# Optimization experiments

Hardware: AMD Instinct MI355X
Metric: run time of the kernel (lower is better)

## Reference

```python
import jax, jax.numpy as jnp
import numpy as np

WORD_THRES = 0.2
COS_EPS = 1e-8
NEG_INF = -1e9


def setup_inputs() -> dict:
    key = jax.random.key(0)
    k1, k2, k3, k4 = jax.random.split(key, 4)
    B, L, V, E, A = 1024, 256, 50000, 300, 30
    inputs = jax.random.randint(k1, (B, L), 0, V)            # token ids, 0 == pad
    w_emb = jax.random.normal(k2, (V, E), dtype=jnp.float32) * 0.1
    a_emb = jax.random.normal(k3, (A, E), dtype=jnp.float32)
    a_weight = jax.random.uniform(k4, (A,), dtype=jnp.float32)
    return {"inputs": inputs, "w_emb": w_emb, "a_emb": a_emb, "a_weight": a_weight}


def reference(inputs, w_emb, a_emb, a_weight):
    # inputs: [B, L] int ids; w_emb: [V, E]; a_emb: [A, E]; a_weight: [A]
    inputs_len = (inputs != 0).sum(axis=1).astype(jnp.float32)      # [B]
    x_wrd = w_emb[inputs]                                            # [B, L, E]

    # cosine similarity between each aspect and each word (torch semantics:
    # dot / (max(||a||, eps) * max(||x||, eps)))
    a_norm = jnp.maximum(jnp.linalg.norm(a_emb, axis=-1), COS_EPS)   # [A]
    x_norm = jnp.maximum(jnp.linalg.norm(x_wrd, axis=-1), COS_EPS)   # [B, L]
    dot = jnp.einsum("ae,ble->abl", a_emb, x_wrd)                    # [A, B, L]
    sim = dot / (a_norm[:, None, None] * x_norm[None, :, :])

    # Threshold(word_thres, 0): x if x > thres else 0, then scale by aspect weight
    sim = jnp.where(sim > WORD_THRES, sim, 0.0) * a_weight[:, None, None]

    # centroid score: relu(sim).max over aspects, summed over seq, length-normalized
    centroid = jnp.maximum(sim, 0.0).max(axis=0)                     # [B, L]
    centroid_score = centroid.sum(axis=1) / (inputs_len + 1e-5)      # [B]

    # attention: mask exact zeros to -1e9, max over aspects, softmax over seq
    sim_m = jnp.where(sim == 0.0, NEG_INF, sim)
    scores = sim_m.max(axis=0)                                       # [B, L]
    a = jax.nn.softmax(scores, axis=1)                               # [B, L]

    z = jnp.einsum("bl,ble->be", a, x_wrd)                           # [B, E]
    enc_out = z * (centroid_score > 1e-4).astype(z.dtype)[:, None]
    return enc_out, a, centroid_score
```

## Files before the change

### kernel.cpp

```cpp
#include <hip/hip_runtime.h>
#include <math.h>

#define BB 1024
#define LL 256
#define VV 50000
#define EE 300
#define AA 30
#define WORD_THRES 0.2f
#define COS_EPS_F 1e-8f
#define NEG_INF_F -1e9f
#define RECHECK_DELTA 2e-4f

typedef __attribute__((ext_vector_type(8))) short bf16x8;
typedef __attribute__((ext_vector_type(4))) float f32x4;

#define MFMA16(a, b, c) __builtin_amdgcn_mfma_f32_16x16x32_bf16((a), (b), (c), 0, 0, 0)

__device__ __forceinline__ void gld_lds16(const float* g, float* l) {
    typedef const __attribute__((address_space(1))) void* gas_p;
    typedef __attribute__((address_space(3))) void* las_p;
    __builtin_amdgcn_global_load_lds((gas_p)g, (las_p)l, 16, 0, 0);
}

__device__ __forceinline__ unsigned pack_hi(float a, float b) {
    return (__float_as_uint(a) >> 16) | (__float_as_uint(b) & 0xFFFF0000u);
}
__device__ __forceinline__ float hi_part(float a) {
    return __uint_as_float(__float_as_uint(a) & 0xFFFF0000u);
}
__device__ __forceinline__ void cvt_hilo(const float4 f0, const float4 f1,
                                         uint4& uh, uint4& ul) {
    uh.x = pack_hi(f0.x, f0.y);
    uh.y = pack_hi(f0.z, f0.w);
    uh.z = pack_hi(f1.x, f1.y);
    uh.w = pack_hi(f1.z, f1.w);
    const float l0 = f0.x - hi_part(f0.x), l1 = f0.y - hi_part(f0.y);
    const float l2 = f0.z - hi_part(f0.z), l3 = f0.w - hi_part(f0.w);
    const float l4 = f1.x - hi_part(f1.x), l5 = f1.y - hi_part(f1.y);
    const float l6 = f1.z - hi_part(f1.z), l7 = f1.w - hi_part(f1.w);
    ul.x = pack_hi(l0, l1);
    ul.y = pack_hi(l2, l3);
    ul.z = pack_hi(l4, l5);
    ul.w = pack_hi(l6, l7);
}

__global__ void __launch_bounds__(128) cent_kernel(
    const float* __restrict__ w_emb,
    const float* __restrict__ a_emb,
    const float* __restrict__ a_weight,
    float* __restrict__ cent)
{
    __shared__ float4 s_a4[2400];
    __shared__ uint4 s_bfrag[40 * 64];
    __shared__ float s_scale[32];
    __shared__ float s_aw[32];

    const int t = threadIdx.x;
    const int l = t & 63;
    const int w = t >> 6;
    const int m = l & 15;
    const int kg = l >> 4;
    float* s_af = (float*)s_a4;

    {
        const float* gbase = w_emb + (size_t)blockIdx.x * 32 * EE;
        const float* gend = w_emb + (size_t)VV * EE;
#pragma unroll
        for (int i = 0; i < 19; ++i) {
            if (i < 18 || t < 96) {
                const int off = i * 512 + t * 4;
                const float* src = gbase + off;
                if (src > gend - 4) src = gend - 4;
                gld_lds16(src, s_af + off);
            }
        }
    }

    {
        const int a = t >> 2, j = t & 3;
        if (a < AA) {
            const float4* a4 = (const float4*)a_emb + a * 75;
            float n2a = 0.f;
            for (int c = j; c < 75; c += 4) {
                const float4 x = a4[c];
                n2a += x.x * x.x + x.y * x.y + x.z * x.z + x.w * x.w;
            }
            n2a += __shfl_xor(n2a, 1);
            n2a += __shfl_xor(n2a, 2);
            if (j == 0) {
                s_scale[a] = 1.f / fmaxf(sqrtf(n2a), COS_EPS_F);
                s_aw[a] = a_weight[a];
            }
        }
        if (t == 30 || t == 31) { s_scale[t] = 0.f; s_aw[t] = 0.f; }
    }

    for (int ks = w; ks < 10; ks += 2) {
        const int kb = kg * 8 + 32 * ks;
#pragma unroll
        for (int tt = 0; tt < 2; ++tt) {
            const int col = tt * 16 + m;
            float4 f0 = {0.f, 0.f, 0.f, 0.f}, f1 = {0.f, 0.f, 0.f, 0.f};
            if (col < AA) {
                const float* ap = a_emb + col * EE;
                if (kb <= 296) f0 = *(const float4*)(ap + kb);
                if (kb <= 292) f1 = *(const float4*)(ap + kb + 4);
            }
            uint4 uh, ul;
            cvt_hilo(f0, f1, uh, ul);
            s_bfrag[(ks * 4 + tt * 2 + 0) * 64 + l] = uh;
            s_bfrag[(ks * 4 + tt * 2 + 1) * 64 + l] = ul;
        }
    }

    asm volatile("s_waitcnt vmcnt(0)" ::: "memory");
    __syncthreads();

    const int vtile = blockIdx.x * 32 + w * 16;
    const float* __restrict__ arow = s_af + (w * 16 + m) * EE;

    f32x4 acc0 = {0.f, 0.f, 0.f, 0.f};
    f32x4 acc1 = {0.f, 0.f, 0.f, 0.f};
    float n2 = 0.f;
    const uint4* __restrict__ bp0 = s_bfrag + l;

#pragma unroll
    for (int i = 0; i < 10; ++i) {
        const int kb = kg * 8 + 32 * i;
        float4 f0 = *(const float4*)(arow + kb);
        float4 f1 = *(const float4*)(arow + kb + 4);
        if (i == 9) {
            const float4 z = {0.f, 0.f, 0.f, 0.f};
            if (kg >= 2) f0 = z;
            if (kg >= 1) f1 = z;
        }
        n2 = fmaf(f0.x, f0.x, fmaf(f0.y, f0.y, fmaf(f0.z, f0.z, fmaf(f0.w, f0.w, n2))));
        n2 = fmaf(f1.x, f1.x, fmaf(f1.y, f1.y, fmaf(f1.z, f1.z, fmaf(f1.w, f1.w, n2))));
        uint4 uh, ul;
        cvt_hilo(f0, f1, uh, ul);
        const bf16x8 ah = __builtin_bit_cast(bf16x8, uh);
        const bf16x8 al = __builtin_bit_cast(bf16x8, ul);
        const uint4* bp = bp0 + i * 256;
        const bf16x8 bh0 = __builtin_bit_cast(bf16x8, bp[0]);
        const bf16x8 bl0 = __builtin_bit_cast(bf16x8, bp[64]);
        const bf16x8 bh1 = __builtin_bit_cast(bf16x8, bp[128]);
        const bf16x8 bl1 = __builtin_bit_cast(bf16x8, bp[192]);
        acc0 = MFMA16(ah, bh0, acc0);
        acc1 = MFMA16(ah, bh1, acc1);
        acc0 = MFMA16(ah, bl0, acc0);
        acc1 = MFMA16(ah, bl1, acc1);
        acc0 = MFMA16(al, bh0, acc0);
        acc1 = MFMA16(al, bh1, acc1);
    }

    n2 += __shfl_xor(n2, 16);
    n2 += __shfl_xor(n2, 32);

    const float sc0 = s_scale[m], aw0 = s_aw[m];
    const float sc1 = s_scale[16 + m], aw1 = s_aw[16 + m];
    const bool col1ok = (16 + m) < AA;
    float mx[4];
#pragma unroll
    for (int j = 0; j < 4; ++j) {
        const int r = kg * 4 + j;
        const float n2r = __int_as_float(
            __builtin_amdgcn_ds_bpermute(r << 2, __float_as_int(n2)));
        const float inv_x = 1.f / fmaxf(sqrtf(n2r), COS_EPS_F);
        float c0 = acc0[j] * sc0 * inv_x;
        float c1 = acc1[j] * sc1 * inv_x;
        if (fabsf(c0 - WORD_THRES) < RECHECK_DELTA) {
            const float* wr = s_af + (w * 16 + r) * EE;
            const float* ar = a_emb + m * EE;
            float d = 0.f;
            for (int k = 0; k < EE; ++k) d = fmaf(wr[k], ar[k], d);
            c0 = d * sc0 * inv_x;
        }
        if (col1ok && fabsf(c1 - WORD_THRES) < RECHECK_DELTA) {
            const float* wr = s_af + (w * 16 + r) * EE;
            const float* ar = a_emb + (16 + m) * EE;
            float d = 0.f;
            for (int k = 0; k < EE; ++k) d = fmaf(wr[k], ar[k], d);
            c1 = d * sc1 * inv_x;
        }
        float mj = fmaxf((c0 > WORD_THRES) ? c0 * aw0 : 0.f,
                         (c1 > WORD_THRES) ? c1 * aw1 : 0.f);
        mj = fmaxf(mj, __shfl_xor(mj, 1));
        mj = fmaxf(mj, __shfl_xor(mj, 2));
        mj = fmaxf(mj, __shfl_xor(mj, 4));
        mj = fmaxf(mj, __shfl_xor(mj, 8));
        mx[j] = mj;
    }
    if (m == 0 && vtile < VV) {
        const float4 o = {mx[0], mx[1], mx[2], mx[3]};
        *(float4*)(cent + vtile + kg * 4) = o;
    }
}

__global__ void __launch_bounds__(256) row_kernel(
    const int* __restrict__ inputs,
    const float* __restrict__ w_emb,
    const float* __restrict__ cent,
    float* __restrict__ out)
{
    const int w = threadIdx.x >> 6;
    const int lane = threadIdx.x & 63;
    const int b = blockIdx.x * 4 + w;

    __shared__ int s_id[4][LL];
    __shared__ float s_w[4][LL];
    __shared__ int s_n[4];

    if (lane == 0) s_n[w] = 0;

    const int4 id4 = *(const int4*)(inputs + b * LL + lane * 4);
    const float c0 = cent[id4.x];
    const float c1 = cent[id4.y];
    const float c2 = cent[id4.z];
    const float c3 = cent[id4.w];
    const float sc0 = (c0 > 0.f) ? c0 : NEG_INF_F;
    const float sc1 = (c1 > 0.f) ? c1 : NEG_INF_F;
    const float sc2 = (c2 > 0.f) ? c2 : NEG_INF_F;
    const float sc3 = (c3 > 0.f) ? c3 : NEG_INF_F;

    float s1 = c0 + c1 + c2 + c3;
    float s2 = (id4.x != 0 ? 1.f : 0.f) + (id4.y != 0 ? 1.f : 0.f) +
               (id4.z != 0 ? 1.f : 0.f) + (id4.w != 0 ? 1.f : 0.f);
    float s3 = fmaxf(fmaxf(sc0, sc1), fmaxf(sc2, sc3));
#pragma unroll
    for (int o = 1; o < 64; o <<= 1) {
        s1 += __shfl_xor(s1, o);
        s2 += __shfl_xor(s2, o);
        s3 = fmaxf(s3, __shfl_xor(s3, o));
    }
    const float mx = s3;

    const float p0 = expf(sc0 - mx);
    const float p1 = expf(sc1 - mx);
    const float p2 = expf(sc2 - mx);
    const float p3 = expf(sc3 - mx);
    float s4 = p0 + p1 + p2 + p3;
#pragma unroll
    for (int o = 1; o < 64; o <<= 1) s4 += __shfl_xor(s4, o);

    const float rinv = 1.f / s4;
    const float4 av = {p0 * rinv, p1 * rinv, p2 * rinv, p3 * rinv};
    *(float4*)(out + BB * EE + b * LL + lane * 4) = av;

    const float cs = s1 / (s2 + 1e-5f);
    const float gate = (cs > 1e-4f) ? 1.f : 0.f;
    if (lane == 0) out[BB * EE + BB * LL + b] = cs;

    if (sc0 > -1e8f) { const int i = atomicAdd(&s_n[w], 1); s_id[w][i] = id4.x; s_w[w][i] = av.x; }
    if (sc1 > -1e8f) { const int i = atomicAdd(&s_n[w], 1); s_id[w][i] = id4.y; s_w[w][i] = av.y; }
    if (sc2 > -1e8f) { const int i = atomicAdd(&s_n[w], 1); s_id[w][i] = id4.z; s_w[w][i] = av.z; }
    if (sc3 > -1e8f) { const int i = atomicAdd(&s_n[w], 1); s_id[w][i] = id4.w; s_w[w][i] = av.w; }
    __syncthreads();
    const int n = s_n[w];

    float4 accA = {0.f, 0.f, 0.f, 0.f};
    float4 accB = {0.f, 0.f, 0.f, 0.f};
    for (int i = 0; i < n; ++i) {
        const float wgt = s_w[w][i];
        const float4* rp = (const float4*)(w_emb + (size_t)s_id[w][i] * EE);
        const float4 ra = rp[lane];
        accA.x += wgt * ra.x; accA.y += wgt * ra.y;
        accA.z += wgt * ra.z; accA.w += wgt * ra.w;
        if (lane < 11) {
            const float4 rb = rp[64 + lane];
            accB.x += wgt * rb.x; accB.y += wgt * rb.y;
            accB.z += wgt * rb.z; accB.w += wgt * rb.w;
        }
    }
    accA.x *= gate; accA.y *= gate; accA.z *= gate; accA.w *= gate;
    *(float4*)(out + b * EE + 4 * lane) = accA;
    if (lane < 11) {
        accB.x *= gate; accB.y *= gate; accB.z *= gate; accB.w *= gate;
        *(float4*)(out + b * EE + 256 + 4 * lane) = accB;
    }
}

extern "C" void kernel_launch(void* const* d_in, const int* in_sizes, int n_in,
                              void* d_out, int out_size, void* d_ws, size_t ws_size,
                              hipStream_t stream) {
    const int* inputs = (const int*)d_in[0];
    const float* w_emb = (const float*)d_in[1];
    const float* a_emb = (const float*)d_in[2];
    const float* a_weight = (const float*)d_in[3];
    float* out = (float*)d_out;
    float* cent = (float*)d_ws;

    cent_kernel<<<(VV + 31) / 32, 128, 0, stream>>>(w_emb, a_emb, a_weight, cent);
    row_kernel<<<BB / 4, 256, 0, stream>>>(inputs, w_emb, cent, out);
}
```

Measured before the change: 135.8 us.

## Make centroid kernel persistent with double-buffered LDS staging and register-resident aspect fragments

The centroid kernel becomes a persistent grid of 256 blocks, one per CU, each looping over 64-row vocab tiles. Each wave stages the next tile into a second LDS buffer with async global-to-LDS loads while it computes the current one. The aspect B fragments are converted once and kept in registers, so they are no longer reread from LDS on every tile. This removes per-block launch and setup cost and hides load latency, but leaves only one block per CU and puts heavy pressure on registers and LDS.

```diff
diff --git a/kernel.cpp b/kernel.cpp
--- a/kernel.cpp
+++ b/kernel.cpp
@@ -10,6 +10,8 @@
 #define COS_EPS_F 1e-8f
 #define NEG_INF_F -1e9f
 #define RECHECK_DELTA 2e-4f
+#define CGRID 256
+#define NTILES 782
 
 typedef __attribute__((ext_vector_type(8))) short bf16x8;
 typedef __attribute__((ext_vector_type(4))) float f32x4;
@@ -44,14 +46,29 @@
     ul.w = pack_hi(l6, l7);
 }
 
-__global__ void __launch_bounds__(128) cent_kernel(
+__device__ __forceinline__ void stage16(const float* __restrict__ w_emb,
+                                        int tile, int w, int lane, float* dst) {
+    const float* gend = w_emb + (size_t)VV * EE - 4;
+    const float* g = w_emb + ((size_t)tile * 64 + w * 16) * EE;
+    float* d = dst + w * 4800;
+#pragma unroll
+    for (int i = 0; i < 19; ++i) {
+        if (i < 18 || lane < 48) {
+            const int off = i * 256 + lane * 4;
+            const float* src = g + off;
+            if (src > gend) src = gend;
+            gld_lds16(src, d + off);
+        }
+    }
+}
+
+__global__ void __launch_bounds__(256, 1) cent_kernel(
     const float* __restrict__ w_emb,
     const float* __restrict__ a_emb,
     const float* __restrict__ a_weight,
     float* __restrict__ cent)
 {
-    __shared__ float4 s_a4[2400];
-    __shared__ uint4 s_bfrag[40 * 64];
+    __shared__ uint4 s_pool[9600];
     __shared__ float s_scale[32];
     __shared__ float s_aw[32];
 
@@ -60,33 +77,19 @@
     const int w = t >> 6;
     const int m = l & 15;
     const int kg = l >> 4;
-    float* s_af = (float*)s_a4;
 
     {
-        const float* gbase = w_emb + (size_t)blockIdx.x * 32 * EE;
-        const float* gend = w_emb + (size_t)VV * EE;
-#pragma unroll
-        for (int i = 0; i < 19; ++i) {
-            if (i < 18 || t < 96) {
-                const int off = i * 512 + t * 4;
-                const float* src = gbase + off;
-                if (src > gend - 4) src = gend - 4;
-                gld_lds16(src, s_af + off);
-            }
-        }
-    }
-
-    {
-        const int a = t >> 2, j = t & 3;
+        const int a = t >> 3, j = t & 7;
         if (a < AA) {
             const float4* a4 = (const float4*)a_emb + a * 75;
             float n2a = 0.f;
-            for (int c = j; c < 75; c += 4) {
+            for (int c = j; c < 75; c += 8) {
                 const float4 x = a4[c];
                 n2a += x.x * x.x + x.y * x.y + x.z * x.z + x.w * x.w;
             }
             n2a += __shfl_xor(n2a, 1);
             n2a += __shfl_xor(n2a, 2);
+            n2a += __shfl_xor(n2a, 4);
             if (j == 0) {
                 s_scale[a] = 1.f / fmaxf(sqrtf(n2a), COS_EPS_F);
                 s_aw[a] = a_weight[a];
@@ -95,104 +98,122 @@
         if (t == 30 || t == 31) { s_scale[t] = 0.f; s_aw[t] = 0.f; }
     }
 
-    for (int ks = w; ks < 10; ks += 2) {
-        const int kb = kg * 8 + 32 * ks;
-#pragma unroll
-        for (int tt = 0; tt < 2; ++tt) {
-            const int col = tt * 16 + m;
-            float4 f0 = {0.f, 0.f, 0.f, 0.f}, f1 = {0.f, 0.f, 0.f, 0.f};
-            if (col < AA) {
-                const float* ap = a_emb + col * EE;
-                if (kb <= 296) f0 = *(const float4*)(ap + kb);
-                if (kb <= 292) f1 = *(const float4*)(ap + kb + 4);
-            }
-            uint4 uh, ul;
-            cvt_hilo(f0, f1, uh, ul);
-            s_bfrag[(ks * 4 + tt * 2 + 0) * 64 + l] = uh;
-            s_bfrag[(ks * 4 + tt * 2 + 1) * 64 + l] = ul;
-        }
-    }
-
-    asm volatile("s_waitcnt vmcnt(0)" ::: "memory");
+    {
+        uint4* s_bfrag = s_pool;
+        for (int ks = w; ks < 10; ks += 4) {
+            const int kb = kg * 8 + 32 * ks;
+#pragma unroll
+            for (int tt = 0; tt < 2; ++tt) {
+                const int col = tt * 16 + m;
+                float4 f0 = {0.f, 0.f, 0.f, 0.f}, f1 = {0.f, 0.f, 0.f, 0.f};
+                if (col < AA) {
+                    const float* ap = a_emb + col * EE;
+                    if (kb <= 296) f0 = *(const float4*)(ap + kb);
+                    if (kb <= 292) f1 = *(const float4*)(ap + kb + 4);
+                }
+                uint4 uh, ul;
+                cvt_hilo(f0, f1, uh, ul);
+                s_bfrag[(ks * 4 + tt * 2 + 0) * 64 + l] = uh;
+                s_bfrag[(ks * 4 + tt * 2 + 1) * 64 + l] = ul;
+            }
+        }
+    }
     __syncthreads();
 
-    const int vtile = blockIdx.x * 32 + w * 16;
-    const float* __restrict__ arow = s_af + (w * 16 + m) * EE;
-
-    f32x4 acc0 = {0.f, 0.f, 0.f, 0.f};
-    f32x4 acc1 = {0.f, 0.f, 0.f, 0.f};
-    float n2 = 0.f;
-    const uint4* __restrict__ bp0 = s_bfrag + l;
-
-#pragma unroll
-    for (int i = 0; i < 10; ++i) {
-        const int kb = kg * 8 + 32 * i;
-        float4 f0 = *(const float4*)(arow + kb);
-        float4 f1 = *(const float4*)(arow + kb + 4);
-        if (i == 9) {
-            const float4 z = {0.f, 0.f, 0.f, 0.f};
-            if (kg >= 2) f0 = z;
-            if (kg >= 1) f1 = z;
-        }
-        n2 = fmaf(f0.x, f0.x, fmaf(f0.y, f0.y, fmaf(f0.z, f0.z, fmaf(f0.w, f0.w, n2))));
-        n2 = fmaf(f1.x, f1.x, fmaf(f1.y, f1.y, fmaf(f1.z, f1.z, fmaf(f1.w, f1.w, n2))));
-        uint4 uh, ul;
-        cvt_hilo(f0, f1, uh, ul);
-        const bf16x8 ah = __builtin_bit_cast(bf16x8, uh);
-        const bf16x8 al = __builtin_bit_cast(bf16x8, ul);
-        const uint4* bp = bp0 + i * 256;
-        const bf16x8 bh0 = __builtin_bit_cast(bf16x8, bp[0]);
-        const bf16x8 bl0 = __builtin_bit_cast(bf16x8, bp[64]);
-        const bf16x8 bh1 = __builtin_bit_cast(bf16x8, bp[128]);
-        const bf16x8 bl1 = __builtin_bit_cast(bf16x8, bp[192]);
-        acc0 = MFMA16(ah, bh0, acc0);
-        acc1 = MFMA16(ah, bh1, acc1);
-        acc0 = MFMA16(ah, bl0, acc0);
-        acc1 = MFMA16(ah, bl1, acc1);
-        acc0 = MFMA16(al, bh0, acc0);
-        acc1 = MFMA16(al, bh1, acc1);
-    }
-
-    n2 += __shfl_xor(n2, 16);
-    n2 += __shfl_xor(n2, 32);
+    bf16x8 bfr[40];
+#pragma unroll
+    for (int q = 0; q < 40; ++q)
+        bfr[q] = __builtin_bit_cast(bf16x8, s_pool[q * 64 + l]);
+    __syncthreads();
+
+    float* buf0 = (float*)s_pool;
+    float* buf1 = buf0 + 19200;
 
     const float sc0 = s_scale[m], aw0 = s_aw[m];
     const float sc1 = s_scale[16 + m], aw1 = s_aw[16 + m];
     const bool col1ok = (16 + m) < AA;
-    float mx[4];
-#pragma unroll
-    for (int j = 0; j < 4; ++j) {
-        const int r = kg * 4 + j;
-        const float n2r = __int_as_float(
-            __builtin_amdgcn_ds_bpermute(r << 2, __float_as_int(n2)));
-        const float inv_x = 1.f / fmaxf(sqrtf(n2r), COS_EPS_F);
-        float c0 = acc0[j] * sc0 * inv_x;
-        float c1 = acc1[j] * sc1 * inv_x;
-        if (fabsf(c0 - WORD_THRES) < RECHECK_DELTA) {
-            const float* wr = s_af + (w * 16 + r) * EE;
-            const float* ar = a_emb + m * EE;
-            float d = 0.f;
-            for (int k = 0; k < EE; ++k) d = fmaf(wr[k], ar[k], d);
-            c0 = d * sc0 * inv_x;
-        }
-        if (col1ok && fabsf(c1 - WORD_THRES) < RECHECK_DELTA) {
-            const float* wr = s_af + (w * 16 + r) * EE;
-            const float* ar = a_emb + (16 + m) * EE;
-            float d = 0.f;
-            for (int k = 0; k < EE; ++k) d = fmaf(wr[k], ar[k], d);
-            c1 = d * sc1 * inv_x;
-        }
-        float mj = fmaxf((c0 > WORD_THRES) ? c0 * aw0 : 0.f,
-                         (c1 > WORD_THRES) ? c1 * aw1 : 0.f);
-        mj = fmaxf(mj, __shfl_xor(mj, 1));
-        mj = fmaxf(mj, __shfl_xor(mj, 2));
-        mj = fmaxf(mj, __shfl_xor(mj, 4));
-        mj = fmaxf(mj, __shfl_xor(mj, 8));
-        mx[j] = mj;
-    }
-    if (m == 0 && vtile < VV) {
-        const float4 o = {mx[0], mx[1], mx[2], mx[3]};
-        *(float4*)(cent + vtile + kg * 4) = o;
+
+    int cur = 0;
+    int tile = blockIdx.x;
+    stage16(w_emb, tile, w, l, buf0);
+
+    for (; tile < NTILES; tile += CGRID) {
+        const int nxt = tile + CGRID;
+        float* bufc = cur ? buf1 : buf0;
+        if (nxt < NTILES) {
+            stage16(w_emb, nxt, w, l, cur ? buf0 : buf1);
+            asm volatile("s_waitcnt vmcnt(19)" ::: "memory");
+        } else {
+            asm volatile("s_waitcnt vmcnt(0)" ::: "memory");
+        }
+
+        const float* arow = bufc + w * 4800 + m * 300;
+        f32x4 acc0 = {0.f, 0.f, 0.f, 0.f};
+        f32x4 acc1 = {0.f, 0.f, 0.f, 0.f};
+        float n2 = 0.f;
+#pragma unroll
+        for (int i = 0; i < 10; ++i) {
+            const int kb = kg * 8 + 32 * i;
+            float4 f0 = *(const float4*)(arow + kb);
+            float4 f1 = *(const float4*)(arow + kb + 4);
+            if (i == 9) {
+                const float4 z = {0.f, 0.f, 0.f, 0.f};
+                if (kg >= 2) f0 = z;
+                if (kg >= 1) f1 = z;
+            }
+            n2 = fmaf(f0.x, f0.x, fmaf(f0.y, f0.y, fmaf(f0.z, f0.z, fmaf(f0.w, f0.w, n2))));
+            n2 = fmaf(f1.x, f1.x, fmaf(f1.y, f1.y, fmaf(f1.z, f1.z, fmaf(f1.w, f1.w, n2))));
+            uint4 uh, ul;
+            cvt_hilo(f0, f1, uh, ul);
+            const bf16x8 ah = __builtin_bit_cast(bf16x8, uh);
+            const bf16x8 al = __builtin_bit_cast(bf16x8, ul);
+            acc0 = MFMA16(ah, bfr[i * 4 + 0], acc0);
+            acc1 = MFMA16(ah, bfr[i * 4 + 2], acc1);
+            acc0 = MFMA16(ah, bfr[i * 4 + 1], acc0);
+            acc1 = MFMA16(ah, bfr[i * 4 + 3], acc1);
+            acc0 = MFMA16(al, bfr[i * 4 + 0], acc0);
+            acc1 = MFMA16(al, bfr[i * 4 + 2], acc1);
+        }
+
+        n2 += __shfl_xor(n2, 16);
+        n2 += __shfl_xor(n2, 32);
+        const int vtile = tile * 64 + w * 16;
+        float mx[4];
+#pragma unroll
+        for (int j = 0; j < 4; ++j) {
+            const int r = kg * 4 + j;
+            const float n2r = __int_as_float(
+                __builtin_amdgcn_ds_bpermute(r << 2, __float_as_int(n2)));
+            const float inv_x = 1.f / fmaxf(sqrtf(n2r), COS_EPS_F);
+            float c0 = acc0[j] * sc0 * inv_x;
+            float c1 = acc1[j] * sc1 * inv_x;
+            if (fabsf(c0 - WORD_THRES) < RECHECK_DELTA) {
+                const float* wr = bufc + w * 4800 + r * 300;
+                const float* ar = a_emb + m * EE;
+                float d = 0.f;
+                for (int k = 0; k < EE; ++k) d = fmaf(wr[k], ar[k], d);
+                c0 = d * sc0 * inv_x;
+            }
+            if (col1ok && fabsf(c1 - WORD_THRES) < RECHECK_DELTA) {
+                const float* wr = bufc + w * 4800 + r * 300;
+                const float* ar = a_emb + (16 + m) * EE;
+                float d = 0.f;
+                for (int k = 0; k < EE; ++k) d = fmaf(wr[k], ar[k], d);
+                c1 = d * sc1 * inv_x;
+            }
+            float mj = fmaxf((c0 > WORD_THRES) ? c0 * aw0 : 0.f,
+                             (c1 > WORD_THRES) ? c1 * aw1 : 0.f);
+            mj = fmaxf(mj, __shfl_xor(mj, 1));
+            mj = fmaxf(mj, __shfl_xor(mj, 2));
+            mj = fmaxf(mj, __shfl_xor(mj, 4));
+            mj = fmaxf(mj, __shfl_xor(mj, 8));
+            mx[j] = mj;
+        }
+        if (m == 0 && vtile < VV) {
+            const float4 o = {mx[0], mx[1], mx[2], mx[3]};
+            *(float4*)(cent + vtile + kg * 4) = o;
+        }
+        cur ^= 1;
     }
 }
 
@@ -289,6 +310,6 @@
     float* out = (float*)d_out;
     float* cent = (float*)d_ws;
 
-    cent_kernel<<<(VV + 31) / 32, 128, 0, stream>>>(w_emb, a_emb, a_weight, cent);
+    cent_kernel<<<CGRID, 256, 0, stream>>>(w_emb, a_emb, a_weight, cent);
     row_kernel<<<BB / 4, 256, 0, stream>>>(inputs, w_emb, cent, out);
 }
```

Result: faster. 115.4 us (-15.1%).
